# Kernel optimization log

Measured on AMD Instinct MI355X. Metric: run time of the kernel, lower is better.

## Reference

```python
import jax, jax.numpy as jnp
import numpy as np

T, B = 128, 4096
TB = T * B
NUM_ACTIONS, N_WORDS, EMB = 6, 16, 16
IMG_FEAT, LOC_DIM, HID = 16, 4, 128
IN_DIM = IMG_FEAT + LOC_DIM + EMB  # 36
GRID_SIZE = 5.0


def setup_inputs() -> dict:
    key = jax.random.key(0)
    ks = jax.random.split(key, 32)
    p = lambda i, shape, s=0.1: (jax.random.normal(ks[i], shape, dtype=jnp.float32) * s)
    inp = {
        'image': jax.random.uniform(ks[0], (TB, 1, 3, 3), dtype=jnp.float32) * 255.0,
        'location': jax.random.uniform(ks[1], (TB, 2), dtype=jnp.float32) * GRID_SIZE,
        'message': jax.random.randint(ks[2], (TB,), 0, N_WORDS, dtype=jnp.int32),
        'done': (jax.random.uniform(ks[3], (TB,)) < 0.05).astype(jnp.float32),
        'h0': p(4, (B, HID)),
        'c0': p(5, (B, HID)),
        # visual encoder 9->256->256->128->16
        'vw1': p(6, (256, 9)), 'vb1': p(7, (256,)),
        'vw2': p(8, (256, 256)), 'vb2': p(9, (256,)),
        'vw3': p(10, (128, 256)), 'vb3': p(11, (128,)),
        'vw4': p(12, (IMG_FEAT, 128)), 'vb4': p(13, (IMG_FEAT,)),
        # message encoder: embedding + linear
        'emb': p(14, (N_WORDS, EMB)),
        'mw': p(15, (EMB, EMB)), 'mb': p(16, (EMB,)),
        # location encoder 2->4
        'lw': p(17, (LOC_DIM, 2)), 'lb': p(18, (LOC_DIM,)),
        # LSTM (PyTorch layout: gates ordered i,f,g,o)
        'w_ih': p(19, (4 * HID, IN_DIM)), 'w_hh': p(20, (4 * HID, HID)),
        'b_ih': p(21, (4 * HID,)), 'b_hh': p(22, (4 * HID,)),
        # heads
        'aw': p(23, (NUM_ACTIONS, HID), 0.01), 'ab': jnp.zeros((NUM_ACTIONS,), jnp.float32),
        'cw': p(24, (1, HID), 1.0), 'cb': jnp.zeros((1,), jnp.float32),
        'msw': p(25, (N_WORDS, HID), 0.01), 'msb': jnp.zeros((N_WORDS,), jnp.float32),
    }
    return inp


def _encode(image, location, message, vw1, vb1, vw2, vb2, vw3, vb3, vw4, vb4,
            emb, mw, mb, lw, lb):
    img = image.reshape(image.shape[0], -1) / 255.0  # [TB, 9]
    h = jax.nn.relu(img @ vw1.T + vb1)
    h = jax.nn.relu(h @ vw2.T + vb2)
    h = jax.nn.relu(h @ vw3.T + vb3)
    img_feat = jax.nn.relu(h @ vw4.T + vb4)           # [TB, 16]
    loc_feat = (location / GRID_SIZE) @ lw.T + lb     # [TB, 4]
    msg_feat = jax.nn.relu(emb[message] @ mw.T + mb)  # [TB, 16]
    return jnp.concatenate([img_feat, loc_feat, msg_feat], axis=1)  # [TB, 36]


def _lstm_scan(x, done, h0, c0, w_ih, w_hh, b_ih, b_hh):
    # x: [T, B, IN], done: [T, B]
    def step(carry, inp):
        h, c = carry
        xt, dt = inp
        mask = (1.0 - dt)[:, None]
        h = h * mask
        c = c * mask
        gates = xt @ w_ih.T + b_ih + h @ w_hh.T + b_hh  # [B, 4H]
        i, f, g, o = jnp.split(gates, 4, axis=1)
        i = jax.nn.sigmoid(i); f = jax.nn.sigmoid(f)
        g = jnp.tanh(g); o = jax.nn.sigmoid(o)
        c = f * c + i * g
        h = o * jnp.tanh(c)
        return (h, c), h
    (hN, cN), hs = jax.lax.scan(step, (h0, c0), (x, done))
    return hs, hN, cN


def reference(image, location, message, done, h0, c0,
              vw1, vb1, vw2, vb2, vw3, vb3, vw4, vb4,
              emb, mw, mb, lw, lb,
              w_ih, w_hh, b_ih, b_hh,
              aw, ab, cw, cb, msw, msb):
    feat = _encode(image, location, message, vw1, vb1, vw2, vb2, vw3, vb3,
                   vw4, vb4, emb, mw, mb, lw, lb)
    x = feat.reshape(T, B, IN_DIM)
    d = done.reshape(T, B)
    hs, hN, cN = _lstm_scan(x, d, h0, c0, w_ih, w_hh, b_ih, b_hh)
    hidden = hs.reshape(TB, HID)
    action_logits = hidden @ aw.T + ab    # [TB, num_actions]
    message_logits = hidden @ msw.T + msb  # [TB, n_words]
    value = hidden @ cw.T + cb            # [TB, 1]
    return hidden, action_logits, message_logits, value, hN, cN
```

## Files before the change

### kernel.cpp

```cpp
#include <hip/hip_runtime.h>
#include <hip/hip_fp16.h>

typedef _Float16 half8 __attribute__((ext_vector_type(8)));
typedef float f32x4 __attribute__((ext_vector_type(4)));

#define MFMA16(a, b, c) __builtin_amdgcn_mfma_f32_16x16x32_f16((a), (b), (c), 0, 0, 0)
#define DEVI __device__ __forceinline__

static constexpr int T_ = 128, B_ = 4096, HID_ = 128;
static constexpr int TB_ = T_ * B_;

static constexpr size_t W1P = 0;
static constexpr size_t W2P = 8192;
static constexpr size_t W3P = 73728;
static constexpr size_t W4P = 106496;
static constexpr size_t WHL = 108544;
static constexpr size_t MSGT = 305152;
static constexpr size_t FEAT = 305408;
static constexpr size_t WS_HALFS = FEAT + (size_t)TB_ * 40;

static constexpr size_t OUT_ACT = (size_t)TB_ * 128;
static constexpr size_t OUT_MSG = OUT_ACT + (size_t)TB_ * 6;
static constexpr size_t OUT_VAL = OUT_MSG + (size_t)TB_ * 16;
static constexpr size_t OUT_HN  = OUT_VAL + (size_t)TB_;
static constexpr size_t OUT_CN  = OUT_HN + (size_t)B_ * 128;

DEVI float sigm_(float x) { return __builtin_amdgcn_rcpf(1.f + __expf(-x)); }
DEVI float tanh_(float x) { return 1.f - 2.f * __builtin_amdgcn_rcpf(1.f + __expf(2.f * x)); }

__global__ void k_pack(const float* __restrict__ src, _Float16* __restrict__ dst,
                       int KT, int srcN, int srcK, int total) {
    int idx = blockIdx.x * 256 + threadIdx.x;
    if (idx >= total) return;
    int j = idx & 7, l = (idx >> 3) & 63, rest = idx >> 9;
    int kt = rest % KT, nt = rest / KT;
    int n = nt * 16 + (l & 15);
    int k = kt * 32 + ((l >> 4) << 3) + j;
    float v = (n < srcN && k < srcK) ? src[n * srcK + k] : 0.f;
    dst[idx] = (_Float16)v;
}

__global__ void k_pack_hilo(const float* __restrict__ wih, const float* __restrict__ whh,
                            _Float16* __restrict__ dst) {
    int idx = blockIdx.x * 256 + threadIdx.x;
    int j = idx & 7, l = (idx >> 3) & 63, rest = idx >> 9;
    int kt = rest % 12, nt = rest / 12;
    int n = nt * 16 + (l & 15);
    int k = (kt % 6) * 32 + ((l >> 4) << 3) + j;
    float v;
    if (k < 64) v = (k < 36) ? wih[n * 36 + k] : 0.f;
    else        v = whh[n * 128 + (k - 64)];
    float hi = (float)(_Float16)v;
    dst[idx] = (kt < 6) ? (_Float16)hi : (_Float16)(v - hi);
}

__global__ void k_misc(const float* __restrict__ emb, const float* __restrict__ mw,
                       const float* __restrict__ mb, const float* __restrict__ bih,
                       const float* __restrict__ bhh, _Float16* __restrict__ msgt,
                       float* __restrict__ bcomb) {
    int t = threadIdx.x;
    if (t < 256) {
        int w = t >> 4, j = t & 15;
        float a = mb[j];
        for (int e = 0; e < 16; ++e) a += emb[w * 16 + e] * mw[j * 16 + e];
        msgt[t] = (_Float16)fmaxf(a, 0.f);
    }
    bcomb[t] = bih[t] + bhh[t];
}

__global__ __launch_bounds__(256, 2)
void k_encoder(const float* __restrict__ img, const float* __restrict__ loc,
               const int* __restrict__ msg,
               const float* __restrict__ vb1, const float* __restrict__ vb2,
               const float* __restrict__ vb3, const float* __restrict__ vb4,
               const float* __restrict__ lw, const float* __restrict__ lb,
               const _Float16* __restrict__ wsh, _Float16* __restrict__ feat) {
    __shared__ __align__(16) _Float16 sA[64 * 40];
    __shared__ __align__(16) _Float16 sU[64 * 264];
    __shared__ __align__(16) _Float16 sV[64 * 264];
    __shared__ int smsg[64];

    const int tid = threadIdx.x;
    const int lane = tid & 63, wv = tid >> 6;
    const int lq = lane >> 4, lr = lane & 15;
    const int rowbase = blockIdx.x * 64;

    for (int i = tid; i < 576; i += 256) {
        int m = i / 9, k = i - m * 9;
        sA[m * 40 + k] = (_Float16)(img[(size_t)rowbase * 9 + i] * (1.f / 255.f));
    }
    for (int i = tid; i < 64 * 32; i += 256) {
        int m = i >> 5, k = 9 + (i & 31);
        if (k < 40) sA[m * 40 + k] = (_Float16)0.f;
    }
    if (tid < 64) smsg[tid] = msg[rowbase + tid];
    __syncthreads();

    const half8* w1p = (const half8*)(wsh + W1P);
    const half8* w2p = (const half8*)(wsh + W2P);
    const half8* w3p = (const half8*)(wsh + W3P);
    const half8* w4p = (const half8*)(wsh + W4P);

    {
        half8 afr[4];
        #pragma unroll
        for (int mt = 0; mt < 4; ++mt)
            afr[mt] = *(const half8*)&sA[(mt * 16 + lr) * 40 + lq * 8];
        #pragma unroll
        for (int ntl = 0; ntl < 4; ++ntl) {
            const int nt = wv * 4 + ntl;
            half8 bfr = w1p[nt * 64 + lane];
            f32x4 acc[4];
            #pragma unroll
            for (int mt = 0; mt < 4; ++mt) acc[mt] = (f32x4){0.f, 0.f, 0.f, 0.f};
            #pragma unroll
            for (int mt = 0; mt < 4; ++mt) acc[mt] = MFMA16(afr[mt], bfr, acc[mt]);
            const int n = nt * 16 + lr;
            const float bias = vb1[n];
            #pragma unroll
            for (int mt = 0; mt < 4; ++mt)
                #pragma unroll
                for (int r = 0; r < 4; ++r)
                    sU[(mt * 16 + lq * 4 + r) * 264 + n] = (_Float16)fmaxf(acc[mt][r] + bias, 0.f);
        }
    }
    __syncthreads();

    {
        half8 afr[4][8];
        #pragma unroll
        for (int mt = 0; mt < 4; ++mt)
            #pragma unroll
            for (int kt = 0; kt < 8; ++kt)
                afr[mt][kt] = *(const half8*)&sU[(mt * 16 + lr) * 264 + kt * 32 + lq * 8];
        #pragma unroll
        for (int ntl = 0; ntl < 4; ++ntl) {
            const int nt = wv * 4 + ntl;
            half8 bfr[8];
            #pragma unroll
            for (int kt = 0; kt < 8; ++kt) bfr[kt] = w2p[(nt * 8 + kt) * 64 + lane];
            f32x4 acc[4];
            #pragma unroll
            for (int mt = 0; mt < 4; ++mt) acc[mt] = (f32x4){0.f, 0.f, 0.f, 0.f};
            #pragma unroll
            for (int kt = 0; kt < 8; ++kt)
                #pragma unroll
                for (int mt = 0; mt < 4; ++mt)
                    acc[mt] = MFMA16(afr[mt][kt], bfr[kt], acc[mt]);
            const int n = nt * 16 + lr;
            const float bias = vb2[n];
            #pragma unroll
            for (int mt = 0; mt < 4; ++mt)
                #pragma unroll
                for (int r = 0; r < 4; ++r)
                    sV[(mt * 16 + lq * 4 + r) * 264 + n] = (_Float16)fmaxf(acc[mt][r] + bias, 0.f);
        }
    }
    __syncthreads();

    {
        half8 afr[4][8];
        #pragma unroll
        for (int mt = 0; mt < 4; ++mt)
            #pragma unroll
            for (int kt = 0; kt < 8; ++kt)
                afr[mt][kt] = *(const half8*)&sV[(mt * 16 + lr) * 264 + kt * 32 + lq * 8];
        #pragma unroll
        for (int ntl = 0; ntl < 2; ++ntl) {
            const int nt = wv * 2 + ntl;
            half8 bfr[8];
            #pragma unroll
            for (int kt = 0; kt < 8; ++kt) bfr[kt] = w3p[(nt * 8 + kt) * 64 + lane];
            f32x4 acc[4];
            #pragma unroll
            for (int mt = 0; mt < 4; ++mt) acc[mt] = (f32x4){0.f, 0.f, 0.f, 0.f};
            #pragma unroll
            for (int kt = 0; kt < 8; ++kt)
                #pragma unroll
                for (int mt = 0; mt < 4; ++mt)
                    acc[mt] = MFMA16(afr[mt][kt], bfr[kt], acc[mt]);
            const int n = nt * 16 + lr;
            const float bias = vb3[n];
            #pragma unroll
            for (int mt = 0; mt < 4; ++mt)
                #pragma unroll
                for (int r = 0; r < 4; ++r)
                    sU[(mt * 16 + lq * 4 + r) * 264 + n] = (_Float16)fmaxf(acc[mt][r] + bias, 0.f);
        }
    }
    __syncthreads();

    {
        half8 b4[4], a4[4];
        #pragma unroll
        for (int kt = 0; kt < 4; ++kt) {
            b4[kt] = w4p[kt * 64 + lane];
            a4[kt] = *(const half8*)&sU[(wv * 16 + lr) * 264 + kt * 32 + lq * 8];
        }
        f32x4 acc = (f32x4){0.f, 0.f, 0.f, 0.f};
        #pragma unroll
        for (int kt = 0; kt < 4; ++kt) acc = MFMA16(a4[kt], b4[kt], acc);
        const float bias = vb4[lr];
        #pragma unroll
        for (int r = 0; r < 4; ++r)
            sA[(wv * 16 + lq * 4 + r) * 40 + lr] = (_Float16)fmaxf(acc[r] + bias, 0.f);
    }

    {
        int m = tid >> 2, o = tid & 3;
        float x0 = loc[(size_t)(rowbase + m) * 2 + 0] * 0.2f;
        float x1 = loc[(size_t)(rowbase + m) * 2 + 1] * 0.2f;
        sA[m * 40 + 16 + o] = (_Float16)(x0 * lw[o * 2 + 0] + x1 * lw[o * 2 + 1] + lb[o]);
    }
    {
        const _Float16* mst = wsh + MSGT;
        for (int f = tid; f < 1024; f += 256) {
            int m = f >> 4, c = f & 15;
            sA[m * 40 + 20 + c] = mst[smsg[m] * 16 + c];
        }
    }
    {
        int m = tid >> 2, c = 36 + (tid & 3);
        sA[m * 40 + c] = (_Float16)0.f;
    }
    __syncthreads();

    uint4* dst = (uint4*)(feat + (size_t)rowbase * 40);
    const uint4* srcv = (const uint4*)sA;
    for (int i = tid; i < 320; i += 256) dst[i] = srcv[i];
}

__global__ __attribute__((amdgpu_flat_work_group_size(512, 512)))
__attribute__((amdgpu_waves_per_eu(2, 2)))
void k_lstm8(const _Float16* __restrict__ wsh, const float* __restrict__ bcomb,
             const float* __restrict__ done, const float* __restrict__ h0,
             const float* __restrict__ c0, float* __restrict__ hid,
             float* __restrict__ hN, float* __restrict__ cN) {
    __shared__ __align__(16) _Float16 sH[2][16 * 136];
    __shared__ __align__(16) _Float16 sX[2][16 * 72];
    __shared__ __align__(16) float sDm[2][16];

    const int tid = threadIdx.x;
    const int w = tid >> 6, lane = tid & 63;
    const int lq = lane >> 4, lr = lane & 15;
    const int b0 = blockIdx.x * 16;
    const int j = w * 16 + lr;
    const _Float16* feat = wsh + FEAT;
    const half8* wlt = (const half8*)(wsh + WHL);

    half8 wfr[4][12];
    #pragma unroll
    for (int g = 0; g < 4; ++g)
        #pragma unroll
        for (int kt = 0; kt < 12; ++kt)
            wfr[g][kt] = wlt[((8 * g + w) * 12 + kt) * 64 + lane];

    float bias[4];
    #pragma unroll
    for (int g = 0; g < 4; ++g) bias[g] = bcomb[g * 128 + j];

    f32x4 cc, hl;
    #pragma unroll
    for (int r = 0; r < 4; ++r) cc[r] = c0[(size_t)(b0 + lq * 4 + r) * 128 + j];

    for (int i = tid; i < 2048; i += 512) {
        int m = i >> 7, k = i & 127;
        sH[0][m * 136 + k] = (_Float16)h0[(size_t)(b0 + m) * 128 + k];
    }
    for (int i = tid; i < 1024; i += 512) {
        int bb = i >> 9, rem = i & 511;
        int m = rem >> 5, c = 40 + (rem & 31);
        sX[bb][m * 72 + c] = (_Float16)0.f;
    }
    const bool stx = tid < 160;
    const int sm = tid / 10, sc = tid - sm * 10;
    if (stx) *(uint2*)(&sX[0][sm * 72 + sc * 4]) =
        *(const uint2*)(feat + (size_t)(b0 + sm) * 40 + sc * 4);
    if (tid < 16) sDm[0][tid] = 1.f - done[b0 + tid];
    __syncthreads();

    const _Float16* fptr = feat + ((size_t)B_ + b0 + sm) * 40 + sc * 4;
    const float* dptr = done + B_ + b0 + tid;
    float* hq = hid + (size_t)b0 * 128 + j;

    for (int t = 0; t < T_; ++t) {
        const int p = t & 1;
        const bool pf = (t + 1 < T_);

        uint2 xreg;
        float dreg;
        if (stx && pf) xreg = *(const uint2*)fptr;
        if (tid < 16 && pf) dreg = dptr[0];
        fptr += (size_t)B_ * 40;
        dptr += B_;

        if (t > 0) {
            #pragma unroll
            for (int r = 0; r < 4; ++r)
                hq[(size_t)(lq * 4 + r) * 128] = hl[r];
            hq += (size_t)B_ * 128;
        }

        const f32x4 dmv = *(const f32x4*)&sDm[p][lq * 4];

        f32x4 acc[4];
        #pragma unroll
        for (int g = 0; g < 4; ++g) acc[g] = (f32x4){0.f, 0.f, 0.f, 0.f};
        #pragma unroll
        for (int u = 0; u < 4; ++u) {
            half8 av = *(const half8*)&sH[p][lr * 136 + u * 32 + lq * 8];
            #pragma unroll
            for (int g = 0; g < 4; ++g) acc[g] = MFMA16(av, wfr[g][2 + u], acc[g]);
            #pragma unroll
            for (int g = 0; g < 4; ++g) acc[g] = MFMA16(av, wfr[g][8 + u], acc[g]);
        }

        if (stx && pf) *(uint2*)(&sX[1 - p][sm * 72 + sc * 4]) = xreg;
        if (tid < 16 && pf) sDm[1 - p][tid] = 1.f - dreg;

        #pragma unroll
        for (int g = 0; g < 4; ++g)
            #pragma unroll
            for (int r = 0; r < 4; ++r)
                acc[g][r] = acc[g][r] * dmv[r] + bias[g];
        {
            half8 x0 = *(const half8*)&sX[p][lr * 72 + lq * 8];
            half8 x1 = *(const half8*)&sX[p][lr * 72 + 32 + lq * 8];
            #pragma unroll
            for (int g = 0; g < 4; ++g) acc[g] = MFMA16(x0, wfr[g][0], acc[g]);
            #pragma unroll
            for (int g = 0; g < 4; ++g) acc[g] = MFMA16(x0, wfr[g][6], acc[g]);
            #pragma unroll
            for (int g = 0; g < 4; ++g) acc[g] = MFMA16(x1, wfr[g][1], acc[g]);
            #pragma unroll
            for (int g = 0; g < 4; ++g) acc[g] = MFMA16(x1, wfr[g][7], acc[g]);
        }

        #pragma unroll
        for (int r = 0; r < 4; ++r) {
            const int m = lq * 4 + r;
            float iv = sigm_(acc[0][r]);
            float fv = sigm_(acc[1][r]);
            float gv = tanh_(acc[2][r]);
            float ov = sigm_(acc[3][r]);
            float cn = fv * (cc[r] * dmv[r]) + iv * gv;
            float hv = ov * tanh_(cn);
            cc[r] = cn;
            hl[r] = hv;
            sH[1 - p][m * 136 + j] = (_Float16)hv;
        }

        __syncthreads();
    }

    #pragma unroll
    for (int r = 0; r < 4; ++r) {
        hq[(size_t)(lq * 4 + r) * 128] = hl[r];
        hN[(size_t)(b0 + lq * 4 + r) * 128 + j] = hl[r];
        cN[(size_t)(b0 + lq * 4 + r) * 128 + j] = cc[r];
    }
}

__global__ __launch_bounds__(256)
void k_heads(const float* __restrict__ hidden, const float* __restrict__ aw,
             const float* __restrict__ ab, const float* __restrict__ cw,
             const float* __restrict__ cb, const float* __restrict__ msw,
             const float* __restrict__ msb, float* __restrict__ oact,
             float* __restrict__ omsg, float* __restrict__ oval) {
    __shared__ __align__(16) float sW[23 * 132];
    __shared__ float sWb[23];
    __shared__ __align__(16) float sHd[64 * 132];
    const int tid = threadIdx.x;
    const int rowbase = blockIdx.x * 64;

    for (int i = tid; i < 23 * 128; i += 256) {
        int o = i >> 7, k = i & 127;
        float v = (o < 6) ? aw[o * 128 + k] : (o < 22) ? msw[(o - 6) * 128 + k] : cw[k];
        sW[o * 132 + k] = v;
    }
    if (tid < 23) sWb[tid] = (tid < 6) ? ab[tid] : (tid < 22) ? msb[tid - 6] : cb[0];
    for (int i = tid; i < 8192; i += 256) {
        int m = i >> 7, k = i & 127;
        sHd[m * 132 + k] = hidden[(size_t)rowbase * 128 + i];
    }
    __syncthreads();

    for (int f = tid; f < 64 * 23; f += 256) {
        int m = f / 23, o = f - m * 23;
        const float* hp = &sHd[m * 132];
        const float* wp = &sW[o * 132];
        f32x4 av = (f32x4){0.f, 0.f, 0.f, 0.f};
        #pragma unroll
        for (int k = 0; k < 128; k += 4)
            av += (*(const f32x4*)(hp + k)) * (*(const f32x4*)(wp + k));
        float acc = sWb[o] + av[0] + av[1] + av[2] + av[3];
        int row = rowbase + m;
        if (o < 6)       oact[(size_t)row * 6 + o] = acc;
        else if (o < 22) omsg[(size_t)row * 16 + (o - 6)] = acc;
        else             oval[row] = acc;
    }
}

extern "C" void kernel_launch(void* const* d_in, const int* in_sizes, int n_in,
                              void* d_out, int out_size, void* d_ws, size_t ws_size,
                              hipStream_t stream) {
    const float* image = (const float*)d_in[0];
    const float* location = (const float*)d_in[1];
    const int*   message = (const int*)d_in[2];
    const float* done = (const float*)d_in[3];
    const float* h0 = (const float*)d_in[4];
    const float* c0 = (const float*)d_in[5];
    const float* vw1 = (const float*)d_in[6];  const float* vb1 = (const float*)d_in[7];
    const float* vw2 = (const float*)d_in[8];  const float* vb2 = (const float*)d_in[9];
    const float* vw3 = (const float*)d_in[10]; const float* vb3 = (const float*)d_in[11];
    const float* vw4 = (const float*)d_in[12]; const float* vb4 = (const float*)d_in[13];
    const float* emb = (const float*)d_in[14];
    const float* mw = (const float*)d_in[15];  const float* mb = (const float*)d_in[16];
    const float* lw = (const float*)d_in[17];  const float* lb = (const float*)d_in[18];
    const float* wih = (const float*)d_in[19]; const float* whh = (const float*)d_in[20];
    const float* bih = (const float*)d_in[21]; const float* bhh = (const float*)d_in[22];
    const float* aw = (const float*)d_in[23];  const float* ab = (const float*)d_in[24];
    const float* cw = (const float*)d_in[25];  const float* cb = (const float*)d_in[26];
    const float* msw = (const float*)d_in[27]; const float* msb = (const float*)d_in[28];

    _Float16* wsh = (_Float16*)d_ws;
    float* bcomb = (float*)((char*)d_ws + WS_HALFS * 2);

    float* out = (float*)d_out;
    float* oh   = out;
    float* oact = out + OUT_ACT;
    float* omsg = out + OUT_MSG;
    float* oval = out + OUT_VAL;
    float* ohN  = out + OUT_HN;
    float* ocN  = out + OUT_CN;

    k_pack<<<32, 256, 0, stream>>>(vw1, wsh + W1P, 1, 256, 9, 8192);
    k_pack<<<256, 256, 0, stream>>>(vw2, wsh + W2P, 8, 256, 256, 65536);
    k_pack<<<128, 256, 0, stream>>>(vw3, wsh + W3P, 8, 128, 256, 32768);
    k_pack<<<8, 256, 0, stream>>>(vw4, wsh + W4P, 4, 16, 128, 2048);
    k_pack_hilo<<<768, 256, 0, stream>>>(wih, whh, wsh + WHL);
    k_misc<<<1, 512, 0, stream>>>(emb, mw, mb, bih, bhh, wsh + MSGT, bcomb);

    k_encoder<<<TB_ / 64, 256, 0, stream>>>(image, location, message, vb1, vb2, vb3, vb4,
                                            lw, lb, wsh, wsh + FEAT);
    k_lstm8<<<B_ / 16, 512, 0, stream>>>(wsh, bcomb, done, h0, c0, oh, ohN, ocN);
    k_heads<<<TB_ / 64, 256, 0, stream>>>(oh, aw, ab, cw, cb, msw, msb, oact, omsg, oval);
}
```

Baseline: 543.0 us.

## Overlap input-projection MFMAs with barrier by loading x into registers directly

The LSTM recurrence kernel no longer stages the per-step input features and done mask through shared memory. Each lane now loads its x fragments and mask values straight from global memory into registers, one step ahead. The input-projection MFMAs, with bias folded into the accumulator init, are issued before the step barrier so they can overlap the wait. The done mask is applied ahead of time to the stored h and c for the next step rather than scaling the accumulated products, which removes a per-element multiply pass. The trade-off is more redundant global loads per lane and a barrier that moves to mid-step, which may change the pipelining behaviour.

```diff
diff --git a/kernel.cpp b/kernel.cpp
--- a/kernel.cpp
+++ b/kernel.cpp
@@ -237,8 +237,6 @@
              const float* __restrict__ c0, float* __restrict__ hid,
              float* __restrict__ hN, float* __restrict__ cN) {
     __shared__ __align__(16) _Float16 sH[2][16 * 136];
-    __shared__ __align__(16) _Float16 sX[2][16 * 72];
-    __shared__ __align__(16) float sDm[2][16];
 
     const int tid = threadIdx.x;
     const int w = tid >> 6, lane = tid & 63;
@@ -259,41 +257,64 @@
     #pragma unroll
     for (int g = 0; g < 4; ++g) bias[g] = bcomb[g * 128 + j];
 
-    f32x4 cc, hl;
-    #pragma unroll
-    for (int r = 0; r < 4; ++r) cc[r] = c0[(size_t)(b0 + lq * 4 + r) * 128 + j];
-
-    for (int i = tid; i < 2048; i += 512) {
-        int m = i >> 7, k = i & 127;
-        sH[0][m * 136 + k] = (_Float16)h0[(size_t)(b0 + m) * 128 + k];
-    }
-    for (int i = tid; i < 1024; i += 512) {
-        int bb = i >> 9, rem = i & 511;
-        int m = rem >> 5, c = 40 + (rem & 31);
-        sX[bb][m * 72 + c] = (_Float16)0.f;
-    }
-    const bool stx = tid < 160;
-    const int sm = tid / 10, sc = tid - sm * 10;
-    if (stx) *(uint2*)(&sX[0][sm * 72 + sc * 4]) =
-        *(const uint2*)(feat + (size_t)(b0 + sm) * 40 + sc * 4);
-    if (tid < 16) sDm[0][tid] = 1.f - done[b0 + tid];
-    __syncthreads();
-
-    const _Float16* fptr = feat + ((size_t)B_ + b0 + sm) * 40 + sc * 4;
-    const float* dptr = done + B_ + b0 + tid;
+    const half8 hz = {0, 0, 0, 0, 0, 0, 0, 0};
+
+    f32x4 cc, hl, ccu;
+    {
+        f32x4 dm0;
+        #pragma unroll
+        for (int r = 0; r < 4; ++r) dm0[r] = 1.f - done[b0 + lq * 4 + r];
+        #pragma unroll
+        for (int r = 0; r < 4; ++r)
+            cc[r] = c0[(size_t)(b0 + lq * 4 + r) * 128 + j] * dm0[r];
+        for (int i = tid; i < 2048; i += 512) {
+            int m = i >> 7, k = i & 127;
+            float d = 1.f - done[b0 + m];
+            sH[0][m * 136 + k] = (_Float16)(h0[(size_t)(b0 + m) * 128 + k] * d);
+        }
+    }
+
+    const _Float16* fx0 = feat + ((size_t)b0 + lr) * 40 + lq * 8;
+    const _Float16* fx1 = feat + ((size_t)b0 + lr) * 40 + 32;
+    half8 xc0 = *(const half8*)fx0;
+    half8 xc1 = (lq == 0) ? *(const half8*)fx1 : hz;
+    fx0 += (size_t)B_ * 40;
+    fx1 += (size_t)B_ * 40;
+
+    const float* dnp = done + (size_t)B_ + b0 + lq * 4;
     float* hq = hid + (size_t)b0 * 128 + j;
+
+    __syncthreads();
 
     for (int t = 0; t < T_; ++t) {
         const int p = t & 1;
         const bool pf = (t + 1 < T_);
 
-        uint2 xreg;
-        float dreg;
-        if (stx && pf) xreg = *(const uint2*)fptr;
-        if (tid < 16 && pf) dreg = dptr[0];
-        fptr += (size_t)B_ * 40;
-        dptr += B_;
-
+        f32x4 acc[4];
+        #pragma unroll
+        for (int g = 0; g < 4; ++g) acc[g] = (f32x4){bias[g], bias[g], bias[g], bias[g]};
+        #pragma unroll
+        for (int g = 0; g < 4; ++g) acc[g] = MFMA16(xc0, wfr[g][0], acc[g]);
+        #pragma unroll
+        for (int g = 0; g < 4; ++g) acc[g] = MFMA16(xc0, wfr[g][6], acc[g]);
+        #pragma unroll
+        for (int g = 0; g < 4; ++g) acc[g] = MFMA16(xc1, wfr[g][1], acc[g]);
+        #pragma unroll
+        for (int g = 0; g < 4; ++g) acc[g] = MFMA16(xc1, wfr[g][7], acc[g]);
+
+        __syncthreads();
+
+        half8 xn0 = hz, xn1 = hz;
+        f32x4 dnext = (f32x4){1.f, 1.f, 1.f, 1.f};
+        if (pf) {
+            xn0 = *(const half8*)fx0;
+            if (lq == 0) xn1 = *(const half8*)fx1;
+            #pragma unroll
+            for (int r = 0; r < 4; ++r) dnext[r] = 1.f - dnp[r];
+        }
+        fx0 += (size_t)B_ * 40;
+        fx1 += (size_t)B_ * 40;
+        dnp += B_;
         if (t > 0) {
             #pragma unroll
             for (int r = 0; r < 4; ++r)
@@ -301,40 +322,26 @@
             hq += (size_t)B_ * 128;
         }
 
-        const f32x4 dmv = *(const f32x4*)&sDm[p][lq * 4];
-
-        f32x4 acc[4];
-        #pragma unroll
-        for (int g = 0; g < 4; ++g) acc[g] = (f32x4){0.f, 0.f, 0.f, 0.f};
-        #pragma unroll
-        for (int u = 0; u < 4; ++u) {
-            half8 av = *(const half8*)&sH[p][lr * 136 + u * 32 + lq * 8];
-            #pragma unroll
-            for (int g = 0; g < 4; ++g) acc[g] = MFMA16(av, wfr[g][2 + u], acc[g]);
-            #pragma unroll
-            for (int g = 0; g < 4; ++g) acc[g] = MFMA16(av, wfr[g][8 + u], acc[g]);
-        }
-
-        if (stx && pf) *(uint2*)(&sX[1 - p][sm * 72 + sc * 4]) = xreg;
-        if (tid < 16 && pf) sDm[1 - p][tid] = 1.f - dreg;
-
-        #pragma unroll
-        for (int g = 0; g < 4; ++g)
-            #pragma unroll
-            for (int r = 0; r < 4; ++r)
-                acc[g][r] = acc[g][r] * dmv[r] + bias[g];
-        {
-            half8 x0 = *(const half8*)&sX[p][lr * 72 + lq * 8];
-            half8 x1 = *(const half8*)&sX[p][lr * 72 + 32 + lq * 8];
-            #pragma unroll
-            for (int g = 0; g < 4; ++g) acc[g] = MFMA16(x0, wfr[g][0], acc[g]);
-            #pragma unroll
-            for (int g = 0; g < 4; ++g) acc[g] = MFMA16(x0, wfr[g][6], acc[g]);
-            #pragma unroll
-            for (int g = 0; g < 4; ++g) acc[g] = MFMA16(x1, wfr[g][1], acc[g]);
-            #pragma unroll
-            for (int g = 0; g < 4; ++g) acc[g] = MFMA16(x1, wfr[g][7], acc[g]);
-        }
+        half8 av0 = *(const half8*)&sH[p][lr * 136 + 0 * 32 + lq * 8];
+        half8 av1 = *(const half8*)&sH[p][lr * 136 + 1 * 32 + lq * 8];
+        half8 av2 = *(const half8*)&sH[p][lr * 136 + 2 * 32 + lq * 8];
+        half8 av3 = *(const half8*)&sH[p][lr * 136 + 3 * 32 + lq * 8];
+        #pragma unroll
+        for (int g = 0; g < 4; ++g) acc[g] = MFMA16(av0, wfr[g][2], acc[g]);
+        #pragma unroll
+        for (int g = 0; g < 4; ++g) acc[g] = MFMA16(av0, wfr[g][8], acc[g]);
+        #pragma unroll
+        for (int g = 0; g < 4; ++g) acc[g] = MFMA16(av1, wfr[g][3], acc[g]);
+        #pragma unroll
+        for (int g = 0; g < 4; ++g) acc[g] = MFMA16(av1, wfr[g][9], acc[g]);
+        #pragma unroll
+        for (int g = 0; g < 4; ++g) acc[g] = MFMA16(av2, wfr[g][4], acc[g]);
+        #pragma unroll
+        for (int g = 0; g < 4; ++g) acc[g] = MFMA16(av2, wfr[g][10], acc[g]);
+        #pragma unroll
+        for (int g = 0; g < 4; ++g) acc[g] = MFMA16(av3, wfr[g][5], acc[g]);
+        #pragma unroll
+        for (int g = 0; g < 4; ++g) acc[g] = MFMA16(av3, wfr[g][11], acc[g]);
 
         #pragma unroll
         for (int r = 0; r < 4; ++r) {
@@ -343,21 +350,22 @@
             float fv = sigm_(acc[1][r]);
             float gv = tanh_(acc[2][r]);
             float ov = sigm_(acc[3][r]);
-            float cn = fv * (cc[r] * dmv[r]) + iv * gv;
+            float cn = fv * cc[r] + iv * gv;
             float hv = ov * tanh_(cn);
-            cc[r] = cn;
+            ccu[r] = cn;
             hl[r] = hv;
-            sH[1 - p][m * 136 + j] = (_Float16)hv;
-        }
-
-        __syncthreads();
+            cc[r] = cn * dnext[r];
+            sH[1 - p][m * 136 + j] = (_Float16)(hv * dnext[r]);
+        }
+        xc0 = xn0;
+        xc1 = xn1;
     }
 
     #pragma unroll
     for (int r = 0; r < 4; ++r) {
         hq[(size_t)(lq * 4 + r) * 128] = hl[r];
         hN[(size_t)(b0 + lq * 4 + r) * 128 + j] = hl[r];
-        cN[(size_t)(b0 + lq * 4 + r) * 128 + j] = cc[r];
+        cN[(size_t)(b0 + lq * 4 + r) * 128 + j] = ccu[r];
     }
 }
 
```

Result: slower. 598.4 us (+10.2%).

## Merge weight-prep kernels, prefetch LSTM inputs two steps ahead, split hi/lo accumulators

Applied to the files above, without the earlier changes.

Six small weight-packing and bias kernels are merged into a single k_prep launch, removing launch gaps between them. In the LSTM recurrence, the x and done prefetch now runs two timesteps ahead through register double-buffering. The shared-memory store for step t+1 happens at the top of the iteration, so global load latency overlaps a full step instead of only the recurrent MFMA block. The hi and lo weight MFMA chains also get separate accumulators, breaking one serial dependency chain into two, at the cost of more registers.

```diff
diff --git a/kernel.cpp b/kernel.cpp
--- a/kernel.cpp
+++ b/kernel.cpp
@@ -28,9 +28,8 @@
 DEVI float sigm_(float x) { return __builtin_amdgcn_rcpf(1.f + __expf(-x)); }
 DEVI float tanh_(float x) { return 1.f - 2.f * __builtin_amdgcn_rcpf(1.f + __expf(2.f * x)); }
 
-__global__ void k_pack(const float* __restrict__ src, _Float16* __restrict__ dst,
-                       int KT, int srcN, int srcK, int total) {
-    int idx = blockIdx.x * 256 + threadIdx.x;
+DEVI void pack_one(const float* __restrict__ src, _Float16* __restrict__ dst,
+                   int KT, int srcN, int srcK, int total, int idx) {
     if (idx >= total) return;
     int j = idx & 7, l = (idx >> 3) & 63, rest = idx >> 9;
     int kt = rest % KT, nt = rest / KT;
@@ -40,32 +39,42 @@
     dst[idx] = (_Float16)v;
 }
 
-__global__ void k_pack_hilo(const float* __restrict__ wih, const float* __restrict__ whh,
-                            _Float16* __restrict__ dst) {
-    int idx = blockIdx.x * 256 + threadIdx.x;
-    int j = idx & 7, l = (idx >> 3) & 63, rest = idx >> 9;
-    int kt = rest % 12, nt = rest / 12;
-    int n = nt * 16 + (l & 15);
-    int k = (kt % 6) * 32 + ((l >> 4) << 3) + j;
-    float v;
-    if (k < 64) v = (k < 36) ? wih[n * 36 + k] : 0.f;
-    else        v = whh[n * 128 + (k - 64)];
-    float hi = (float)(_Float16)v;
-    dst[idx] = (kt < 6) ? (_Float16)hi : (_Float16)(v - hi);
-}
-
-__global__ void k_misc(const float* __restrict__ emb, const float* __restrict__ mw,
+__global__ void k_prep(const float* __restrict__ vw1, const float* __restrict__ vw2,
+                       const float* __restrict__ vw3, const float* __restrict__ vw4,
+                       const float* __restrict__ wih, const float* __restrict__ whh,
+                       const float* __restrict__ emb, const float* __restrict__ mw,
                        const float* __restrict__ mb, const float* __restrict__ bih,
-                       const float* __restrict__ bhh, _Float16* __restrict__ msgt,
+                       const float* __restrict__ bhh, _Float16* __restrict__ wsh,
                        float* __restrict__ bcomb) {
-    int t = threadIdx.x;
-    if (t < 256) {
-        int w = t >> 4, j = t & 15;
+    const int blk = blockIdx.x, tid = threadIdx.x;
+    if (blk < 768) {
+        int idx = blk * 256 + tid;
+        int j = idx & 7, l = (idx >> 3) & 63, rest = idx >> 9;
+        int kt = rest % 12, nt = rest / 12;
+        int n = nt * 16 + (l & 15);
+        int k = (kt % 6) * 32 + ((l >> 4) << 3) + j;
+        float v;
+        if (k < 64) v = (k < 36) ? wih[n * 36 + k] : 0.f;
+        else        v = whh[n * 128 + (k - 64)];
+        float hi = (float)(_Float16)v;
+        wsh[WHL + idx] = (kt < 6) ? (_Float16)hi : (_Float16)(v - hi);
+    } else if (blk < 800) {
+        pack_one(vw1, wsh + W1P, 1, 256, 9, 8192, (blk - 768) * 256 + tid);
+    } else if (blk < 1056) {
+        pack_one(vw2, wsh + W2P, 8, 256, 256, 65536, (blk - 800) * 256 + tid);
+    } else if (blk < 1184) {
+        pack_one(vw3, wsh + W3P, 8, 128, 256, 32768, (blk - 1056) * 256 + tid);
+    } else if (blk < 1192) {
+        pack_one(vw4, wsh + W4P, 4, 16, 128, 2048, (blk - 1184) * 256 + tid);
+    } else if (blk == 1192) {
+        int w = tid >> 4, j = tid & 15;
         float a = mb[j];
         for (int e = 0; e < 16; ++e) a += emb[w * 16 + e] * mw[j * 16 + e];
-        msgt[t] = (_Float16)fmaxf(a, 0.f);
-    }
-    bcomb[t] = bih[t] + bhh[t];
+        wsh[MSGT + tid] = (_Float16)fmaxf(a, 0.f);
+    } else {
+        int i = (blk - 1193) * 256 + tid;
+        bcomb[i] = bih[i] + bhh[i];
+    }
 }
 
 __global__ __launch_bounds__(256, 2)
@@ -277,20 +286,28 @@
     if (stx) *(uint2*)(&sX[0][sm * 72 + sc * 4]) =
         *(const uint2*)(feat + (size_t)(b0 + sm) * 40 + sc * 4);
     if (tid < 16) sDm[0][tid] = 1.f - done[b0 + tid];
-    __syncthreads();
-
-    const _Float16* fptr = feat + ((size_t)B_ + b0 + sm) * 40 + sc * 4;
-    const float* dptr = done + B_ + b0 + tid;
+
+    uint2 xrA = {0, 0}, xrB = {0, 0};
+    float drA = 0.f, drB = 0.f;
+    if (stx) xrA = *(const uint2*)(feat + ((size_t)B_ + b0 + sm) * 40 + sc * 4);
+    if (tid < 16) drA = done[(size_t)B_ + b0 + tid];
+
+    const _Float16* fptr = feat + ((size_t)2 * B_ + b0 + sm) * 40 + sc * 4;
+    const float* dptr = done + (size_t)2 * B_ + b0 + tid;
     float* hq = hid + (size_t)b0 * 128 + j;
+
+    __syncthreads();
 
     for (int t = 0; t < T_; ++t) {
         const int p = t & 1;
-        const bool pf = (t + 1 < T_);
-
-        uint2 xreg;
-        float dreg;
-        if (stx && pf) xreg = *(const uint2*)fptr;
-        if (tid < 16 && pf) dreg = dptr[0];
+        const bool pf1 = (t + 1 < T_);
+        const bool pf2 = (t + 2 < T_);
+
+        if (stx && pf1) *(uint2*)(&sX[1 - p][sm * 72 + sc * 4]) = xrA;
+        if (tid < 16 && pf1) sDm[1 - p][tid] = 1.f - drA;
+
+        if (stx && pf2) xrB = *(const uint2*)fptr;
+        if (tid < 16 && pf2) drB = dptr[0];
         fptr += (size_t)B_ * 40;
         dptr += B_;
 
@@ -303,26 +320,28 @@
 
         const f32x4 dmv = *(const f32x4*)&sDm[p][lq * 4];
 
-        f32x4 acc[4];
-        #pragma unroll
-        for (int g = 0; g < 4; ++g) acc[g] = (f32x4){0.f, 0.f, 0.f, 0.f};
+        f32x4 aH[4], aL[4];
+        #pragma unroll
+        for (int g = 0; g < 4; ++g) {
+            aH[g] = (f32x4){0.f, 0.f, 0.f, 0.f};
+            aL[g] = (f32x4){0.f, 0.f, 0.f, 0.f};
+        }
         #pragma unroll
         for (int u = 0; u < 4; ++u) {
             half8 av = *(const half8*)&sH[p][lr * 136 + u * 32 + lq * 8];
             #pragma unroll
-            for (int g = 0; g < 4; ++g) acc[g] = MFMA16(av, wfr[g][2 + u], acc[g]);
-            #pragma unroll
-            for (int g = 0; g < 4; ++g) acc[g] = MFMA16(av, wfr[g][8 + u], acc[g]);
-        }
-
-        if (stx && pf) *(uint2*)(&sX[1 - p][sm * 72 + sc * 4]) = xreg;
-        if (tid < 16 && pf) sDm[1 - p][tid] = 1.f - dreg;
-
+            for (int g = 0; g < 4; ++g) aH[g] = MFMA16(av, wfr[g][2 + u], aH[g]);
+            #pragma unroll
+            for (int g = 0; g < 4; ++g) aL[g] = MFMA16(av, wfr[g][8 + u], aL[g]);
+        }
+
+        f32x4 acc[4];
         #pragma unroll
         for (int g = 0; g < 4; ++g)
             #pragma unroll
             for (int r = 0; r < 4; ++r)
-                acc[g][r] = acc[g][r] * dmv[r] + bias[g];
+                acc[g][r] = (aH[g][r] + aL[g][r]) * dmv[r] + bias[g];
+
         {
             half8 x0 = *(const half8*)&sX[p][lr * 72 + lq * 8];
             half8 x1 = *(const half8*)&sX[p][lr * 72 + 32 + lq * 8];
@@ -351,6 +370,8 @@
         }
 
         __syncthreads();
+        xrA = xrB;
+        drA = drB;
     }
 
     #pragma unroll
@@ -434,13 +455,8 @@
     float* ohN  = out + OUT_HN;
     float* ocN  = out + OUT_CN;
 
-    k_pack<<<32, 256, 0, stream>>>(vw1, wsh + W1P, 1, 256, 9, 8192);
-    k_pack<<<256, 256, 0, stream>>>(vw2, wsh + W2P, 8, 256, 256, 65536);
-    k_pack<<<128, 256, 0, stream>>>(vw3, wsh + W3P, 8, 128, 256, 32768);
-    k_pack<<<8, 256, 0, stream>>>(vw4, wsh + W4P, 4, 16, 128, 2048);
-    k_pack_hilo<<<768, 256, 0, stream>>>(wih, whh, wsh + WHL);
-    k_misc<<<1, 512, 0, stream>>>(emb, mw, mb, bih, bhh, wsh + MSGT, bcomb);
-
+    k_prep<<<1195, 256, 0, stream>>>(vw1, vw2, vw3, vw4, wih, whh, emb, mw, mb,
+                                     bih, bhh, wsh, bcomb);
     k_encoder<<<TB_ / 64, 256, 0, stream>>>(image, location, message, vb1, vb2, vb3, vb4,
                                             lw, lb, wsh, wsh + FEAT);
     k_lstm8<<<B_ / 16, 512, 0, stream>>>(wsh, bcomb, done, h0, c0, oh, ohN, ocN);
```

Result: slower. 608.2 us (+12.0%).
